# Kernel optimization log

Measured on AMD Instinct MI355X. Metric: run time of the kernel, lower is better.

## Reference

```python
import jax, jax.numpy as jnp
import numpy as np

B, S, D = 2, 2048, 4096
H, KVH, HD = 32, 8, 128
MULT = 0.08838834764831845  # 1/sqrt(head_dim)
MAXV = 30.0                 # tanh soft-cap
ROPE_BASE = 10000.0


def _rope_cos_sin(position_ids, hd=HD, base=ROPE_BASE):
    inv_freq = 1.0 / (base ** (jnp.arange(0, hd, 2, dtype=jnp.float32) / hd))
    freqs = position_ids.astype(jnp.float32)[..., None] * inv_freq  # [B,S,hd/2]
    emb = jnp.concatenate([freqs, freqs], axis=-1)                  # [B,S,hd]
    return jnp.cos(emb), jnp.sin(emb)


def _rotate_half(x):
    half = x.shape[-1] // 2
    return jnp.concatenate([-x[..., half:], x[..., :half]], axis=-1)


def setup_inputs() -> dict:
    key = jax.random.key(0)
    ks = jax.random.split(key, 5)
    hidden_states = jax.random.normal(ks[0], (B, S, D), dtype=jnp.float32)
    position_ids = jnp.broadcast_to(jnp.arange(S, dtype=jnp.int64), (B, S))
    # True = masked (causal upper triangle)
    causal = jnp.triu(jnp.ones((S, S), dtype=bool), k=1)
    attention_mask = jnp.broadcast_to(causal, (B, 1, S, S))
    sc = 0.02
    q_w = jax.random.normal(ks[1], (D, H * HD), dtype=jnp.float32) * sc
    k_w = jax.random.normal(ks[2], (D, KVH * HD), dtype=jnp.float32) * sc
    v_w = jax.random.normal(ks[3], (D, KVH * HD), dtype=jnp.float32) * sc
    o_w = jax.random.normal(ks[4], (H * HD, D), dtype=jnp.float32) * sc
    return {"hidden_states": hidden_states, "position_ids": position_ids,
            "attention_mask": attention_mask, "q_w": q_w, "k_w": k_w,
            "v_w": v_w, "o_w": o_w}


def reference(hidden_states, position_ids, attention_mask, q_w, k_w, v_w, o_w):
    bsz, q_len, _ = hidden_states.shape
    q = (hidden_states @ q_w).reshape(bsz, q_len, H, HD).transpose(0, 2, 1, 3)    # [B,H,S,HD]
    k = (hidden_states @ k_w).reshape(bsz, q_len, KVH, HD).transpose(0, 2, 1, 3)  # [B,KVH,S,HD]
    v = (hidden_states @ v_w).reshape(bsz, q_len, KVH, HD).transpose(0, 2, 1, 3)

    cos, sin = _rope_cos_sin(position_ids)   # [B,S,HD]
    cos = cos[:, None]                       # [B,1,S,HD]
    sin = sin[:, None]
    q = q * cos + _rotate_half(q) * sin
    k = k * cos + _rotate_half(k) * sin

    groups = H // KVH
    k = jnp.repeat(k, groups, axis=1)        # [B,H,S,HD]
    v = jnp.repeat(v, groups, axis=1)

    scores = jnp.einsum('bhqd,bhkd->bhqk', q, k).astype(jnp.float32) * MULT
    scores = MAXV * jnp.tanh(scores / MAXV)
    scores = jnp.where(attention_mask, jnp.float32(-10000.0), scores)
    attn = jax.nn.softmax(scores, axis=-1).astype(q.dtype)

    out = jnp.einsum('bhqk,bhkd->bhqd', attn, v)       # [B,H,S,HD]
    out = out.transpose(0, 2, 1, 3).reshape(bsz, q_len, H * HD)
    return out @ o_w
```

## Files before the change

### kernel.cpp

```cpp
#include <hip/hip_runtime.h>
#include <stdint.h>

#define B_ 2
#define S_ 2048
#define D_ 4096
#define H_ 32
#define KVH_ 8
#define HD_ 128
#define GRP_ (H_/KVH_)
#define NQKV 6144
#define MULT_ 0.08838834764831845f
#define MAXV_ 30.0f

typedef __attribute__((ext_vector_type(8))) short s16x8;
typedef __attribute__((ext_vector_type(4))) float fx4;

__device__ __forceinline__ unsigned short f2bf(float f) {
  unsigned int u = __float_as_uint(f);
  u += 0x7fffu + ((u >> 16) & 1u);
  return (unsigned short)(u >> 16);
}
__device__ __forceinline__ float bf2f(unsigned short h) {
  return __uint_as_float(((unsigned int)h) << 16);
}
__device__ __forceinline__ uint32_t pk2(float lo, float hi) {
  return ((uint32_t)f2bf(hi) << 16) | (uint32_t)f2bf(lo);
}

__device__ __forceinline__ void gld_lds16(const void* g, void* l) {
  __builtin_amdgcn_global_load_lds(
      (const __attribute__((address_space(1))) unsigned int*)g,
      (__attribute__((address_space(3))) unsigned int*)l, 16, 0, 0);
}


__global__ void k_f2bf(const float* __restrict__ src, unsigned short* __restrict__ dst, int n4) {
  int i = blockIdx.x * blockDim.x + threadIdx.x;
  int stride = gridDim.x * blockDim.x;
  for (; i < n4; i += stride) {
    float4 v = ((const float4*)src)[i];
    ushort4 o;
    o.x = f2bf(v.x); o.y = f2bf(v.y); o.z = f2bf(v.z); o.w = f2bf(v.w);
    ((ushort4*)dst)[i] = o;
  }
}

__global__ void k_transpose_w(const float* __restrict__ src, int ncols,
                              unsigned short* __restrict__ dst) {
  __shared__ float tile[32][33];
  int k0 = blockIdx.x * 32;
  int n0 = blockIdx.y * 32;
  int tx = threadIdx.x, ty = threadIdx.y;
  for (int i = 0; i < 32; i += 8)
    tile[ty + i][tx] = src[(size_t)(k0 + ty + i) * ncols + n0 + tx];
  __syncthreads();
  for (int i = 0; i < 32; i += 8)
    dst[(size_t)(n0 + ty + i) * 4096 + k0 + tx] = f2bf(tile[tx][ty + i]);
}

__global__ void k_transpose_v(const unsigned short* __restrict__ qkv,
                              unsigned short* __restrict__ vt) {
  __shared__ unsigned short tile[32][33];
  int s0 = blockIdx.x * 32;
  int d0 = blockIdx.y * 32;
  int bk = blockIdx.z;
  int b = bk / KVH_, kvh = bk % KVH_;
  int tx = threadIdx.x, ty = threadIdx.y;
  for (int i = 0; i < 32; i += 8)
    tile[ty + i][tx] = qkv[(size_t)(b*S_ + s0 + ty + i)*NQKV + 5120 + kvh*HD_ + d0 + tx];
  __syncthreads();
  for (int i = 0; i < 32; i += 8)
    vt[((size_t)bk*HD_ + d0 + ty + i)*S_ + s0 + tx] = tile[tx][ty + i];
}

__global__ void k_rope(const unsigned short* __restrict__ qkv,
                       unsigned short* __restrict__ Q, unsigned short* __restrict__ K) {
  int bs = blockIdx.x;
  int b = bs >> 11;
  int s = bs & (S_ - 1);
  __shared__ float cs[64], sn[64];
  int t = threadIdx.x;
  if (t < 64) {
    float inv = __expf(-(float)t * 0.14391156831212787f);
    float fr = (float)s * inv;
    cs[t] = cosf(fr); sn[t] = sinf(fr);
  }
  __syncthreads();
  const unsigned short* row = qkv + (size_t)bs * NQKV;
  for (int i = t; i < H_*HD_; i += 256) {
    int h = i >> 7, d = i & 127;
    float x = bf2f(row[i]);
    float x2, c, si;
    if (d < 64) { x2 = -bf2f(row[h*128 + d + 64]); c = cs[d];    si = sn[d]; }
    else        { x2 =  bf2f(row[h*128 + d - 64]); c = cs[d-64]; si = sn[d-64]; }
    Q[((size_t)(b*H_ + h)*S_ + s)*HD_ + d] = f2bf(x*c + x2*si);
  }
  for (int i = t; i < KVH_*HD_; i += 256) {
    int h = i >> 7, d = i & 127;
    float x = bf2f(row[4096 + i]);
    float x2, c, si;
    if (d < 64) { x2 = -bf2f(row[4096 + h*128 + d + 64]); c = cs[d];    si = sn[d]; }
    else        { x2 =  bf2f(row[4096 + h*128 + d - 64]); c = cs[d-64]; si = sn[d-64]; }
    K[((size_t)(b*KVH_ + h)*S_ + s)*HD_ + d] = f2bf(x*c + x2*si);
  }
}


#define BAR() asm volatile("s_barrier" ::: "memory")
#define SB0() __builtin_amdgcn_sched_barrier(0)

#define STAGE(buf, isB, h, kt) do {                                          \
  const unsigned short* _src = (isB) ? Bt : A;                               \
  size_t _rb = (size_t)(((isB) ? bn : bm)*((isB) ? BN : 256)                 \
                        + (h)*((isB) ? BN/2 : 128));                         \
  _Pragma("unroll") for (int _rr = 0; _rr < ((isB) ? BN/128 : 2); ++_rr) {   \
    int _s = _rr*8 + wv;                                                     \
    gld_lds16(_src + (_rb + (size_t)((_s>>1)*16))*Kd                         \
                   + (size_t)((kt)*64 + (_s&1)*32) + lane_off,               \
              ldsc + (buf)*PBUF + (isB)*32768                                \
                   + (h)*((isB) ? BN*64 : 16384) + _s*1024);                 \
  }                                                                          \
} while (0)

#define LDA(dst, buf, mh) do {                                               \
  _Pragma("unroll") for (int _i = 0; _i < 4; ++_i)                           \
  _Pragma("unroll") for (int _kk = 0; _kk < 2; ++_kk)                        \
    dst[_i*2+_kk] = *(const s16x8*)(ldsc + (buf)*PBUF + wr*16384             \
                    + ((((mh)*4+_i)*2+_kk)*1024) + aswz);                    \
} while (0)

#define LDB(dst, buf, nh) do {                                               \
  _Pragma("unroll") for (int _j = 0; _j < NFR; ++_j)                         \
  _Pragma("unroll") for (int _kk = 0; _kk < 2; ++_kk)                        \
    dst[_j*2+_kk] = *(const s16x8*)(ldsc + (buf)*PBUF + 32768                \
                    + (wc>>1)*(BN*64)                                        \
                    + ((((wc&1)*2*NFR+(nh)*NFR+_j)*2+_kk)*1024) + aswz);     \
} while (0)

#define MFMA_Q(Aa, Bb, MH, NH) do {                                          \
  __builtin_amdgcn_s_setprio(1);                                            \
  _Pragma("unroll") for (int _i = 0; _i < 4; ++_i)                           \
  _Pragma("unroll") for (int _j = 0; _j < NFR; ++_j)                         \
  _Pragma("unroll") for (int _kk = 0; _kk < 2; ++_kk)                        \
    acc[(MH)*4+_i][(NH)*NFR+_j] = __builtin_amdgcn_mfma_f32_16x16x32_bf16(   \
        Aa[_i*2+_kk], Bb[_j*2+_kk], acc[(MH)*4+_i][(NH)*NFR+_j], 0, 0, 0);   \
  __builtin_amdgcn_s_setprio(0);                                            \
} while (0)

template<int OUTF32, int BN>
__global__ __launch_bounds__(512, 2)
void k_gemm8(const unsigned short* __restrict__ A, const unsigned short* __restrict__ Bt,
             void* __restrict__ C, int Kdim, int N, int MB) {
  constexpr int NFR = BN / 128;
  constexpr int PBUF = 32768 + BN * 128;
  __shared__ __align__(16) char ldsbuf[2 * PBUF];
  char* ldsc = ldsbuf;
  const size_t Kd = (size_t)Kdim;
  const int NT = Kdim >> 6;

  auto VMCN = [] {
    if constexpr (BN == 256) asm volatile("s_waitcnt vmcnt(4)" ::: "memory");
    else                     asm volatile("s_waitcnt vmcnt(2)" ::: "memory");
  };

  int nwg = gridDim.x;
  int flat = blockIdx.x;
  int q = nwg >> 3, r8 = nwg & 7, xcd = flat & 7, off = flat >> 3;
  int wg = (xcd < r8 ? xcd*(q+1) : r8*(q+1) + (xcd-r8)*q) + off;
  int bm = wg % MB, bn = wg / MB;

  int tid = threadIdx.x;
  int lane = tid & 63, wv = tid >> 6;
  int wr = wv >> 2, wc = wv & 3;
  int l15 = lane & 15, l4 = lane >> 4;
  const int aswz = (l15 << 6) + ((l4 << 4) ^ ((l15 & 8) ? 32 : 0));
  const size_t lane_off = (size_t)(lane >> 2) * Kd
                        + (size_t)(((lane & 3) << 3) ^ ((lane & 32) >> 1));

  fx4 acc[8][2*NFR] = {};
  s16x8 Afr[8], B0fr[2*NFR], B1fr[2*NFR];

  STAGE(0, 0, 0, 0); STAGE(0, 0, 1, 0);
  STAGE(0, 1, 0, 0); STAGE(0, 1, 1, 0);
  STAGE(1, 1, 0, 1); STAGE(1, 1, 1, 1);
  VMCN();
  BAR();

  for (int t2 = 0; t2 < NT; t2 += 2) {
    int tb1 = t2 + 1;
    int tn0 = t2 + 2; if (tn0 >= NT) tn0 -= NT;
    int tn1 = t2 + 3; if (tn1 >= NT) tn1 -= NT;
    LDA(Afr, 0, 0); LDB(B0fr, 0, 0);
    STAGE(1, 0, 0, tb1);
    BAR();
    MFMA_Q(Afr, B0fr, 0, 0);
    SB0(); BAR();
    LDB(B1fr, 0, 1);
    STAGE(1, 0, 1, tb1);
    BAR();
    MFMA_Q(Afr, B1fr, 0, 1);
    SB0(); BAR();
    LDA(Afr, 0, 1);
    STAGE(0, 1, 0, tn0);
    BAR();
    MFMA_Q(Afr, B1fr, 1, 1);
    SB0(); BAR();
    STAGE(0, 1, 1, tn0);
    BAR();
    MFMA_Q(Afr, B0fr, 1, 0);
    SB0(); VMCN(); BAR();
    LDA(Afr, 1, 0); LDB(B0fr, 1, 0);
    STAGE(0, 0, 0, tn0);
    BAR();
    MFMA_Q(Afr, B0fr, 0, 0);
    SB0(); BAR();
    LDB(B1fr, 1, 1);
    STAGE(0, 0, 1, tn0);
    BAR();
    MFMA_Q(Afr, B1fr, 0, 1);
    SB0(); BAR();
    LDA(Afr, 1, 1);
    STAGE(1, 1, 0, tn1);
    BAR();
    MFMA_Q(Afr, B1fr, 1, 1);
    SB0(); BAR();
    STAGE(1, 1, 1, tn1);
    BAR();
    MFMA_Q(Afr, B0fr, 1, 0);
    SB0(); VMCN(); BAR();
  }

  int m0 = bm*256 + wr*128 + l4*4;
#pragma unroll
  for (int mf = 0; mf < 8; ++mf)
#pragma unroll
    for (int nf = 0; nf < 2*NFR; ++nf)
#pragma unroll
      for (int r = 0; r < 4; ++r) {
        int m = m0 + mf*16 + r;
        int n = bn*BN + (wc>>1)*(BN/2) + ((wc&1)*2*NFR + nf)*16 + l15;
        float v = acc[mf][nf][r];
        if (OUTF32) ((float*)C)[(size_t)m*N + n] = v;
        else ((unsigned short*)C)[(size_t)m*N + n] = f2bf(v);
      }
}


__global__ __launch_bounds__(256)
void k_attn3(const unsigned short* __restrict__ Q, const unsigned short* __restrict__ K,
             const unsigned short* __restrict__ Vt, unsigned short* __restrict__ Aout) {
  __shared__ unsigned short k_lds[2][64*128];
  __shared__ unsigned short v_lds[2][128*64];
  const float C1 = 0.08838834764831845f * 2.0f * 1.4426950408889634f / 30.0f;
  const float C2 = 30.0f * 1.4426950408889634f;
  int tpair = blockIdx.x;
  int bh = blockIdx.y;
  int b = bh >> 5, h = bh & 31;
  int kvh = h >> 2;
  int tid = threadIdx.x, lane = tid & 63, wv = tid >> 6;
  int l15 = lane & 15, l4 = lane >> 4;
  const unsigned short* Qb = Q + (size_t)bh * S_ * HD_;
  const unsigned short* Kb = K + (size_t)(b*KVH_ + kvh) * S_ * HD_;
  const unsigned short* Vb = Vt + (size_t)(b*KVH_ + kvh) * HD_ * S_;

#define STAGE_KV(bufi, kb64) do {                                            \
  _Pragma("unroll") for (int _it = 0; _it < 4; ++_it) {                      \
    int _c = _it*256 + tid;                                                  \
    int _kr = _c >> 4;                                                       \
    int _kd = ((_c & 15) ^ (_kr & 7)) * 8;                                   \
    gld_lds16(&Kb[(size_t)((kb64) + _kr)*HD_ + _kd],                         \
              &k_lds[bufi][_it*2048 + wv*512]);                              \
    int _vd = _c >> 3;                                                       \
    int _vk = ((_c & 7) ^ (_vd & 7)) * 8;                                    \
    gld_lds16(&Vb[(size_t)_vd*S_ + (kb64) + _vk],                            \
              &v_lds[bufi][_it*2048 + wv*512]);                              \
  }                                                                          \
} while (0)

  for (int sp = 0; sp < 2; ++sp) {
    int strip = sp ? (15 - tpair) : tpair;
    int q0 = strip * 128;
    int qbase = q0 + wv * 32;
    s16x8 bq[2][4];
#pragma unroll
    for (int qf = 0; qf < 2; ++qf)
#pragma unroll
      for (int kb = 0; kb < 4; ++kb)
        bq[qf][kb] = *(const s16x8*)&Qb[(size_t)(qbase + qf*16 + l15)*HD_ + kb*32 + l4*8];
    fx4 oacc[2][8] = {};
    float sump[2] = {0.f, 0.f};
    int nt = q0/64 + 2;
    STAGE_KV(0, 0);
    __syncthreads();
    for (int t = 0; t < nt; ++t) {
      int bufi = t & 1;
      int kbase = t*64;
      if (t + 1 < nt) STAGE_KV(bufi^1, (t+1)*64);
      if (kbase <= qbase + 31) {
        fx4 sst[4][2] = {};
        __builtin_amdgcn_s_setprio(1);
#pragma unroll
        for (int nb = 0; nb < 4; ++nb)
#pragma unroll
          for (int kb = 0; kb < 4; ++kb) {
            s16x8 kf = *(const s16x8*)&k_lds[bufi][(nb*16 + l15)*128 +
                                                   (((kb*4 + l4) ^ (l15 & 7)) * 8)];
            sst[nb][0] = __builtin_amdgcn_mfma_f32_16x16x32_bf16(kf, bq[0][kb], sst[nb][0], 0, 0, 0);
            sst[nb][1] = __builtin_amdgcn_mfma_f32_16x16x32_bf16(kf, bq[1][kb], sst[nb][1], 0, 0, 0);
          }
        __builtin_amdgcn_s_setprio(0);
        s16x8 pf[2][2];
#pragma unroll
        for (int qf = 0; qf < 2; ++qf) {
          int qr = qbase + qf*16 + l15;
          float psum = 0.f;
#pragma unroll
          for (int hp = 0; hp < 2; ++hp) {
            uint32_t w[4];
#pragma unroll
            for (int n2 = 0; n2 < 2; ++n2) {
              int nb = hp*2 + n2;
              float pv[4];
#pragma unroll
              for (int r = 0; r < 4; ++r) {
                int kk = kbase + nb*16 + l4*4 + r;
                float sraw = sst[nb][qf][r];
                float e2 = __builtin_amdgcn_exp2f(-fabsf(sraw) * C1);
                float th = (1.f - e2) * __builtin_amdgcn_rcpf(1.f + e2);
                float th_s = __uint_as_float(__float_as_uint(th) |
                                             (__float_as_uint(sraw) & 0x80000000u));
                float p = __builtin_amdgcn_exp2f(th_s * C2 - C2);
                p = (kk <= qr) ? p : 0.f;
                psum += p;
                pv[r] = p;
              }
              w[n2*2]   = pk2(pv[0], pv[1]);
              w[n2*2+1] = pk2(pv[2], pv[3]);
            }
            uint32_t a0x = __shfl_xor((int)w[0], 16), a1x = __shfl_xor((int)w[1], 16);
            uint32_t b0x = __shfl_xor((int)w[2], 16), b1x = __shfl_xor((int)w[3], 16);
            bool up = (l4 & 1);
            uint32_t VA0 = up ? a0x : w[0], VA1 = up ? a1x : w[1];
            uint32_t VA2 = up ? w[0] : a0x, VA3 = up ? w[1] : a1x;
            uint32_t VB0 = up ? b0x : w[2], VB1 = up ? b1x : w[3];
            uint32_t VB2 = up ? w[2] : b0x, VB3 = up ? w[3] : b1x;
            bool lowh = (l4 < 2);
            uint32_t X0 = lowh ? VB0 : VA0, X1 = lowh ? VB1 : VA1;
            uint32_t X2 = lowh ? VB2 : VA2, X3 = lowh ? VB3 : VA3;
            uint32_t Y0 = __shfl_xor((int)X0, 32), Y1 = __shfl_xor((int)X1, 32);
            uint32_t Y2 = __shfl_xor((int)X2, 32), Y3 = __shfl_xor((int)X3, 32);
            union { uint32_t u[4]; s16x8 v; } tw;
            tw.u[0] = (l4 == 0) ? VA0 : (l4 == 3) ? VB0 : Y0;
            tw.u[1] = (l4 == 0) ? VA1 : (l4 == 3) ? VB1 : Y1;
            tw.u[2] = (l4 == 0) ? VA2 : (l4 == 3) ? VB2 : Y2;
            tw.u[3] = (l4 == 0) ? VA3 : (l4 == 3) ? VB3 : Y3;
            pf[qf][hp] = tw.v;
          }
          sump[qf] += psum;
        }
        __builtin_amdgcn_s_setprio(1);
#pragma unroll
        for (int db = 0; db < 8; ++db) {
          int d = db*16 + l15;
#pragma unroll
          for (int hp = 0; hp < 2; ++hp) {
            s16x8 vf = *(const s16x8*)&v_lds[bufi][d*64 + (((hp*4 + l4) ^ (d & 7)) * 8)];
            oacc[0][db] = __builtin_amdgcn_mfma_f32_16x16x32_bf16(vf, pf[0][hp], oacc[0][db], 0, 0, 0);
            oacc[1][db] = __builtin_amdgcn_mfma_f32_16x16x32_bf16(vf, pf[1][hp], oacc[1][db], 0, 0, 0);
          }
        }
        __builtin_amdgcn_s_setprio(0);
      }
      __syncthreads();
    }
#pragma unroll
    for (int qf = 0; qf < 2; ++qf) {
      float s = sump[qf];
      s += __shfl_xor(s, 16);
      s += __shfl_xor(s, 32);
      float rn = __builtin_amdgcn_rcpf(s);
      int qq = qbase + qf*16 + l15;
#pragma unroll
      for (int db = 0; db < 8; ++db) {
        ushort4 o;
        o.x = f2bf(oacc[qf][db][0] * rn);
        o.y = f2bf(oacc[qf][db][1] * rn);
        o.z = f2bf(oacc[qf][db][2] * rn);
        o.w = f2bf(oacc[qf][db][3] * rn);
        *(ushort4*)&Aout[(size_t)(b*S_ + qq)*4096 + h*HD_ + db*16 + l4*4] = o;
      }
    }
  }
#undef STAGE_KV
}


extern "C" void kernel_launch(void* const* d_in, const int* in_sizes, int n_in,
                              void* d_out, int out_size, void* d_ws, size_t ws_size,
                              hipStream_t stream) {
  (void)in_sizes; (void)n_in; (void)out_size; (void)ws_size;
  const float* hidden = (const float*)d_in[0];
  const float* q_w = (const float*)d_in[3];
  const float* k_w = (const float*)d_in[4];
  const float* v_w = (const float*)d_in[5];
  const float* o_w = (const float*)d_in[6];
  char* ws = (char*)d_ws;
  unsigned short* hidden_bf = (unsigned short*)(ws + 0);
  unsigned short* qkv_wt    = (unsigned short*)(ws + 33554432);
  unsigned short* o_wt      = (unsigned short*)(ws + 83886080);
  unsigned short* qkv       = (unsigned short*)(ws + 117440512);
  unsigned short* Qb        = (unsigned short*)(ws + 167772160);
  unsigned short* Kb        = (unsigned short*)(ws + 201326592);
  unsigned short* Vt        = (unsigned short*)(ws + 209715200);
  unsigned short* attn_out  = (unsigned short*)(ws + 218103808);

  dim3 tb(32, 8);
  k_f2bf<<<2048, 256, 0, stream>>>(hidden, hidden_bf, (B_*S_*D_)/4);
  k_transpose_w<<<dim3(128, 128), tb, 0, stream>>>(q_w, 4096, qkv_wt);
  k_transpose_w<<<dim3(128, 32),  tb, 0, stream>>>(k_w, 1024, qkv_wt + (size_t)4096*4096);
  k_transpose_w<<<dim3(128, 32),  tb, 0, stream>>>(v_w, 1024, qkv_wt + (size_t)5120*4096);
  k_transpose_w<<<dim3(128, 128), tb, 0, stream>>>(o_w, 4096, o_wt);
  k_gemm8<0,128><<<dim3(16*48), 512, 0, stream>>>(hidden_bf, qkv_wt, qkv, D_, NQKV, 16);
  k_rope<<<B_*S_, 256, 0, stream>>>(qkv, Qb, Kb);
  k_transpose_v<<<dim3(S_/32, HD_/32, B_*KVH_), tb, 0, stream>>>(qkv, Vt);
  k_attn3<<<dim3(8, B_*H_), 256, 0, stream>>>(Qb, Kb, Vt, attn_out);
  k_gemm8<1,256><<<dim3(16*16), 512, 0, stream>>>(attn_out, o_wt, d_out, D_, D_, 16);
}
```

Baseline: 647.5 us.

## Drop LDS staging in attention; read K/V directly and remap blocks per XCD

The attention kernel no longer double-buffers K/V tiles in shared memory with block-wide barriers. Each wave now loads its K and V fragments straight from global memory in 32-key steps and stops at its own causal limit, which removes the __syncthreads and the idle waves on diagonal tiles. Blocks use a flattened grid, remapped so the query heads sharing a KV head land on the same XCD, aiming to improve L2 reuse of K/V. The cost is extra global/L2 traffic per wave (no sharing across the 4 waves) and exposed load latency with no software prefetch.

```diff
diff --git a/kernel.cpp b/kernel.cpp
--- a/kernel.cpp
+++ b/kernel.cpp
@@ -247,36 +247,24 @@
 
 
 __global__ __launch_bounds__(256)
-void k_attn3(const unsigned short* __restrict__ Q, const unsigned short* __restrict__ K,
+void k_attn4(const unsigned short* __restrict__ Q, const unsigned short* __restrict__ K,
              const unsigned short* __restrict__ Vt, unsigned short* __restrict__ Aout) {
-  __shared__ unsigned short k_lds[2][64*128];
-  __shared__ unsigned short v_lds[2][128*64];
   const float C1 = 0.08838834764831845f * 2.0f * 1.4426950408889634f / 30.0f;
   const float C2 = 30.0f * 1.4426950408889634f;
-  int tpair = blockIdx.x;
-  int bh = blockIdx.y;
-  int b = bh >> 5, h = bh & 31;
-  int kvh = h >> 2;
+  int fid = blockIdx.x;
+  int xcd = fid & 7, idx = fid >> 3;
+  int g = xcd*2 + (idx >> 5);
+  int i = idx & 31;
+  int tpair = i & 7, hlo = i >> 3;
+  int b = g >> 3, kvh = g & 7;
+  int h = kvh*GRP_ + hlo;
+  int bh = b*H_ + h;
   int tid = threadIdx.x, lane = tid & 63, wv = tid >> 6;
   int l15 = lane & 15, l4 = lane >> 4;
   const unsigned short* Qb = Q + (size_t)bh * S_ * HD_;
   const unsigned short* Kb = K + (size_t)(b*KVH_ + kvh) * S_ * HD_;
   const unsigned short* Vb = Vt + (size_t)(b*KVH_ + kvh) * HD_ * S_;
 
-#define STAGE_KV(bufi, kb64) do {                                            \
-  _Pragma("unroll") for (int _it = 0; _it < 4; ++_it) {                      \
-    int _c = _it*256 + tid;                                                  \
-    int _kr = _c >> 4;                                                       \
-    int _kd = ((_c & 15) ^ (_kr & 7)) * 8;                                   \
-    gld_lds16(&Kb[(size_t)((kb64) + _kr)*HD_ + _kd],                         \
-              &k_lds[bufi][_it*2048 + wv*512]);                              \
-    int _vd = _c >> 3;                                                       \
-    int _vk = ((_c & 7) ^ (_vd & 7)) * 8;                                    \
-    gld_lds16(&Vb[(size_t)_vd*S_ + (kb64) + _vk],                            \
-              &v_lds[bufi][_it*2048 + wv*512]);                              \
-  }                                                                          \
-} while (0)
-
   for (int sp = 0; sp < 2; ++sp) {
     int strip = sp ? (15 - tpair) : tpair;
     int q0 = strip * 128;
@@ -289,89 +277,74 @@
         bq[qf][kb] = *(const s16x8*)&Qb[(size_t)(qbase + qf*16 + l15)*HD_ + kb*32 + l4*8];
     fx4 oacc[2][8] = {};
     float sump[2] = {0.f, 0.f};
-    int nt = q0/64 + 2;
-    STAGE_KV(0, 0);
-    __syncthreads();
+    int nt = (qbase >> 5) + 1;
     for (int t = 0; t < nt; ++t) {
-      int bufi = t & 1;
-      int kbase = t*64;
-      if (t + 1 < nt) STAGE_KV(bufi^1, (t+1)*64);
-      if (kbase <= qbase + 31) {
-        fx4 sst[4][2] = {};
-        __builtin_amdgcn_s_setprio(1);
-#pragma unroll
-        for (int nb = 0; nb < 4; ++nb)
-#pragma unroll
-          for (int kb = 0; kb < 4; ++kb) {
-            s16x8 kf = *(const s16x8*)&k_lds[bufi][(nb*16 + l15)*128 +
-                                                   (((kb*4 + l4) ^ (l15 & 7)) * 8)];
-            sst[nb][0] = __builtin_amdgcn_mfma_f32_16x16x32_bf16(kf, bq[0][kb], sst[nb][0], 0, 0, 0);
-            sst[nb][1] = __builtin_amdgcn_mfma_f32_16x16x32_bf16(kf, bq[1][kb], sst[nb][1], 0, 0, 0);
+      int kbase = t*32;
+      s16x8 kf[2][4];
+#pragma unroll
+      for (int nb = 0; nb < 2; ++nb)
+#pragma unroll
+        for (int kb = 0; kb < 4; ++kb)
+          kf[nb][kb] = *(const s16x8*)&Kb[(size_t)(kbase + nb*16 + l15)*HD_ + kb*32 + l4*8];
+      fx4 sst[2][2] = {};
+#pragma unroll
+      for (int nb = 0; nb < 2; ++nb)
+#pragma unroll
+        for (int kb = 0; kb < 4; ++kb) {
+          sst[nb][0] = __builtin_amdgcn_mfma_f32_16x16x32_bf16(kf[nb][kb], bq[0][kb], sst[nb][0], 0, 0, 0);
+          sst[nb][1] = __builtin_amdgcn_mfma_f32_16x16x32_bf16(kf[nb][kb], bq[1][kb], sst[nb][1], 0, 0, 0);
+        }
+      s16x8 pf[2];
+#pragma unroll
+      for (int qf = 0; qf < 2; ++qf) {
+        int qr = qbase + qf*16 + l15;
+        uint32_t w[4];
+        float psum = 0.f;
+#pragma unroll
+        for (int nb = 0; nb < 2; ++nb) {
+          float pv[4];
+#pragma unroll
+          for (int r = 0; r < 4; ++r) {
+            int kk = kbase + nb*16 + l4*4 + r;
+            float sraw = sst[nb][qf][r];
+            float e2 = __builtin_amdgcn_exp2f(-fabsf(sraw) * C1);
+            float th = (1.f - e2) * __builtin_amdgcn_rcpf(1.f + e2);
+            float th_s = __uint_as_float(__float_as_uint(th) |
+                                         (__float_as_uint(sraw) & 0x80000000u));
+            float p = __builtin_amdgcn_exp2f(th_s * C2 - C2);
+            p = (kk <= qr) ? p : 0.f;
+            psum += p;
+            pv[r] = p;
           }
-        __builtin_amdgcn_s_setprio(0);
-        s16x8 pf[2][2];
-#pragma unroll
-        for (int qf = 0; qf < 2; ++qf) {
-          int qr = qbase + qf*16 + l15;
-          float psum = 0.f;
-#pragma unroll
-          for (int hp = 0; hp < 2; ++hp) {
-            uint32_t w[4];
-#pragma unroll
-            for (int n2 = 0; n2 < 2; ++n2) {
-              int nb = hp*2 + n2;
-              float pv[4];
-#pragma unroll
-              for (int r = 0; r < 4; ++r) {
-                int kk = kbase + nb*16 + l4*4 + r;
-                float sraw = sst[nb][qf][r];
-                float e2 = __builtin_amdgcn_exp2f(-fabsf(sraw) * C1);
-                float th = (1.f - e2) * __builtin_amdgcn_rcpf(1.f + e2);
-                float th_s = __uint_as_float(__float_as_uint(th) |
-                                             (__float_as_uint(sraw) & 0x80000000u));
-                float p = __builtin_amdgcn_exp2f(th_s * C2 - C2);
-                p = (kk <= qr) ? p : 0.f;
-                psum += p;
-                pv[r] = p;
-              }
-              w[n2*2]   = pk2(pv[0], pv[1]);
-              w[n2*2+1] = pk2(pv[2], pv[3]);
-            }
-            uint32_t a0x = __shfl_xor((int)w[0], 16), a1x = __shfl_xor((int)w[1], 16);
-            uint32_t b0x = __shfl_xor((int)w[2], 16), b1x = __shfl_xor((int)w[3], 16);
-            bool up = (l4 & 1);
-            uint32_t VA0 = up ? a0x : w[0], VA1 = up ? a1x : w[1];
-            uint32_t VA2 = up ? w[0] : a0x, VA3 = up ? w[1] : a1x;
-            uint32_t VB0 = up ? b0x : w[2], VB1 = up ? b1x : w[3];
-            uint32_t VB2 = up ? w[2] : b0x, VB3 = up ? w[3] : b1x;
-            bool lowh = (l4 < 2);
-            uint32_t X0 = lowh ? VB0 : VA0, X1 = lowh ? VB1 : VA1;
-            uint32_t X2 = lowh ? VB2 : VA2, X3 = lowh ? VB3 : VA3;
-            uint32_t Y0 = __shfl_xor((int)X0, 32), Y1 = __shfl_xor((int)X1, 32);
-            uint32_t Y2 = __shfl_xor((int)X2, 32), Y3 = __shfl_xor((int)X3, 32);
-            union { uint32_t u[4]; s16x8 v; } tw;
-            tw.u[0] = (l4 == 0) ? VA0 : (l4 == 3) ? VB0 : Y0;
-            tw.u[1] = (l4 == 0) ? VA1 : (l4 == 3) ? VB1 : Y1;
-            tw.u[2] = (l4 == 0) ? VA2 : (l4 == 3) ? VB2 : Y2;
-            tw.u[3] = (l4 == 0) ? VA3 : (l4 == 3) ? VB3 : Y3;
-            pf[qf][hp] = tw.v;
-          }
-          sump[qf] += psum;
+          w[nb*2]   = pk2(pv[0], pv[1]);
+          w[nb*2+1] = pk2(pv[2], pv[3]);
         }
-        __builtin_amdgcn_s_setprio(1);
-#pragma unroll
-        for (int db = 0; db < 8; ++db) {
-          int d = db*16 + l15;
-#pragma unroll
-          for (int hp = 0; hp < 2; ++hp) {
-            s16x8 vf = *(const s16x8*)&v_lds[bufi][d*64 + (((hp*4 + l4) ^ (d & 7)) * 8)];
-            oacc[0][db] = __builtin_amdgcn_mfma_f32_16x16x32_bf16(vf, pf[0][hp], oacc[0][db], 0, 0, 0);
-            oacc[1][db] = __builtin_amdgcn_mfma_f32_16x16x32_bf16(vf, pf[1][hp], oacc[1][db], 0, 0, 0);
-          }
-        }
-        __builtin_amdgcn_s_setprio(0);
+        sump[qf] += psum;
+        uint32_t a0x = __shfl_xor((int)w[0], 16), a1x = __shfl_xor((int)w[1], 16);
+        uint32_t b0x = __shfl_xor((int)w[2], 16), b1x = __shfl_xor((int)w[3], 16);
+        bool up = (l4 & 1);
+        uint32_t VA0 = up ? a0x : w[0], VA1 = up ? a1x : w[1];
+        uint32_t VA2 = up ? w[0] : a0x, VA3 = up ? w[1] : a1x;
+        uint32_t VB0 = up ? b0x : w[2], VB1 = up ? b1x : w[3];
+        uint32_t VB2 = up ? w[2] : b0x, VB3 = up ? w[3] : b1x;
+        bool lowh = (l4 < 2);
+        uint32_t X0 = lowh ? VB0 : VA0, X1 = lowh ? VB1 : VA1;
+        uint32_t X2 = lowh ? VB2 : VA2, X3 = lowh ? VB3 : VA3;
+        uint32_t Y0 = __shfl_xor((int)X0, 32), Y1 = __shfl_xor((int)X1, 32);
+        uint32_t Y2 = __shfl_xor((int)X2, 32), Y3 = __shfl_xor((int)X3, 32);
+        union { uint32_t u[4]; s16x8 v; } tw;
+        tw.u[0] = (l4 == 0) ? VA0 : (l4 == 3) ? VB0 : Y0;
+        tw.u[1] = (l4 == 0) ? VA1 : (l4 == 3) ? VB1 : Y1;
+        tw.u[2] = (l4 == 0) ? VA2 : (l4 == 3) ? VB2 : Y2;
+        tw.u[3] = (l4 == 0) ? VA3 : (l4 == 3) ? VB3 : Y3;
+        pf[qf] = tw.v;
       }
-      __syncthreads();
+#pragma unroll
+      for (int db = 0; db < 8; ++db) {
+        s16x8 vf = *(const s16x8*)&Vb[(size_t)(db*16 + l15)*S_ + kbase + l4*8];
+        oacc[0][db] = __builtin_amdgcn_mfma_f32_16x16x32_bf16(vf, pf[0], oacc[0][db], 0, 0, 0);
+        oacc[1][db] = __builtin_amdgcn_mfma_f32_16x16x32_bf16(vf, pf[1], oacc[1][db], 0, 0, 0);
+      }
     }
 #pragma unroll
     for (int qf = 0; qf < 2; ++qf) {
@@ -391,7 +364,6 @@
       }
     }
   }
-#undef STAGE_KV
 }
 
 
@@ -423,6 +395,6 @@
   k_gemm8<0,128><<<dim3(16*48), 512, 0, stream>>>(hidden_bf, qkv_wt, qkv, D_, NQKV, 16);
   k_rope<<<B_*S_, 256, 0, stream>>>(qkv, Qb, Kb);
   k_transpose_v<<<dim3(S_/32, HD_/32, B_*KVH_), tb, 0, stream>>>(qkv, Vt);
-  k_attn3<<<dim3(8, B_*H_), 256, 0, stream>>>(Qb, Kb, Vt, attn_out);
+  k_attn4<<<dim3(512), 256, 0, stream>>>(Qb, Kb, Vt, attn_out);
   k_gemm8<1,256><<<dim3(16*16), 512, 0, stream>>>(attn_out, o_wt, d_out, D_, D_, 16);
 }
```

After: 676.0 us. +4.4%, slower.
